# Optimization experiments

Hardware: AMD Instinct MI355X
Metric: run time of the kernel (lower is better)

Reference implementation:

```python
import jax, jax.numpy as jnp
import numpy as np

PATCH_NUMS = (1, 2, 3, 4, 5, 6, 8, 10, 13, 16)
MAX_PN = 16
N_PHI = 4
RESI_RATIO = 0.5
TOK_T = 1.0  # tokenize_temperature


def _area_matrix(n_in, n_out):
    # F.interpolate(mode='area') == adaptive_avg_pool: equal-weight fractional bins
    M = np.zeros((n_out, n_in), np.float32)
    for i in range(n_out):
        s = (i * n_in) // n_out
        e = -((-(i + 1) * n_in) // n_out)  # ceil
        M[i, s:e] = 1.0 / (e - s)
    return M


def _cubic(t, a=-0.75):
    t = abs(float(t))
    if t <= 1.0:
        return (a + 2) * t ** 3 - (a + 3) * t ** 2 + 1.0
    if t < 2.0:
        return a * t ** 3 - 5 * a * t ** 2 + 8 * a * t - 4 * a
    return 0.0


def _bicubic_matrix(n_in, n_out):
    # PyTorch bicubic, align_corners=False, a=-0.75, edge-clamped taps
    M = np.zeros((n_out, n_in), np.float32)
    scale = n_in / n_out
    for j in range(n_out):
        src = (j + 0.5) * scale - 0.5
        fi = int(np.floor(src))
        t = src - fi
        for k in range(-1, 3):
            idx = min(max(fi + k, 0), n_in - 1)
            M[j, idx] += _cubic(k - t)
    return M


def _resize_sep(x, M):
    # separable spatial resize: x [B,C,H,W] -> [B,C,out,out]
    y = jnp.einsum('ph,bchw->bcpw', M, x)
    return jnp.einsum('qw,bcpw->bcpq', M, y)


def setup_inputs() -> dict:
    key = jax.random.key(0)
    k1, k2, k3 = jax.random.split(key, 3)
    feat = jax.random.normal(k1, (128, 32, 16, 16), jnp.float32)
    codebook = jax.random.normal(k2, (4096, 32), jnp.float32)
    phi_w = jax.random.normal(k3, (N_PHI, 32, 32, 3, 3), jnp.float32) * 0.05
    phi_b = jnp.zeros((N_PHI, 32), jnp.float32)
    return {"feat": feat, "codebook": codebook, "phi_w": phi_w, "phi_b": phi_b}


def reference(feat, codebook, phi_w, phi_b):
    B, C, H, W = feat.shape
    K = len(PATCH_NUMS)
    denom = max(K - 1, 1)
    c2 = jnp.sum(codebook * codebook, axis=-1)  # [V]
    f_rest = feat
    f_hat = jnp.zeros_like(feat)
    contexts = []
    for si, pn in enumerate(PATCH_NUMS):
        if si < K - 1:
            A = jnp.asarray(_area_matrix(H, pn))
            z = _resize_sep(f_rest, A)
        else:
            z = f_rest
        zt = z.transpose(0, 2, 3, 1).reshape(B, pn * pn, C)  # [B, pn^2, C]
        x2 = jnp.sum(zt * zt, axis=-1, keepdims=True)
        logits = -(x2 + c2[None, None, :] - 2.0 * jnp.einsum('bnc,vc->bnv', zt, codebook))
        probs = jax.nn.softmax(logits / max(TOK_T, 1e-6), axis=-1)
        idx = jnp.argmax(probs, axis=-1)
        hard = codebook[idx]                                   # [B, pn^2, C]
        soft = jnp.einsum('bnv,vc->bnc', probs, codebook)
        emb = hard + soft - jax.lax.stop_gradient(soft)        # STE (fwd value == hard)
        h = emb.reshape(B, pn, pn, C).transpose(0, 3, 1, 2)    # [B, C, pn, pn]
        if si < K - 1:
            U = jnp.asarray(_bicubic_matrix(pn, MAX_PN))
            h_up = _resize_sep(h, U)
        else:
            h_up = h
        pi = int(round(si / denom * (N_PHI - 1)))              # quant_resi[si/denom]
        conv = jax.lax.conv_general_dilated(
            h_up, phi_w[pi], (1, 1), 'SAME',
            dimension_numbers=('NCHW', 'OIHW', 'NCHW')) + phi_b[pi][None, :, None, None]
        h_up = h_up * (1.0 - RESI_RATIO) + conv * RESI_RATIO
        f_hat = f_hat + h_up
        f_rest = f_rest - h_up
        if pn < MAX_PN:
            fk = _resize_sep(f_hat, jnp.asarray(_area_matrix(H, pn)))
        else:
            fk = f_hat
        contexts.append(fk.reshape(B, C, pn * pn).transpose(0, 2, 1))  # [B, pn^2, C]
    return jnp.concatenate(contexts, axis=1)  # [B, 680, C]
```

## Files before the change

### kernel.cpp

```cpp
#include <hip/hip_runtime.h>

#define B 128
#define C 32
#define HH 16
#define V 4096
#define MARGIN 1e-4f

typedef __attribute__((ext_vector_type(8))) short bf16x8;
typedef __attribute__((ext_vector_type(4))) float f32x4;


__device__ __forceinline__ float cubicw(float t) {
    float at = fabsf(t);
    float at2 = at * at, at3 = at2 * at;
    if (at <= 1.f) return 1.25f * at3 - 2.25f * at2 + 1.f;
    if (at < 2.f)  return -0.75f * at3 + 3.75f * at2 - 6.f * at + 3.f;
    return 0.f;
}

__device__ __forceinline__ unsigned short f2bf_rne(float f) {
    unsigned int u = __float_as_uint(f);
    unsigned int r = (u + 0x7fffu + ((u >> 16) & 1u)) >> 16;
    return (unsigned short)r;
}
__device__ __forceinline__ float bf2f(unsigned short h) {
    return __uint_as_float(((unsigned int)h) << 16);
}


__global__ void setup_kernel(const float* __restrict__ feat, float* __restrict__ f_rest,
                             float* __restrict__ f_hat, const float* __restrict__ cb,
                             double* __restrict__ c2d, float* __restrict__ c2f,
                             float* __restrict__ z0, unsigned short* __restrict__ cbh,
                             unsigned short* __restrict__ cbl) {
    int i = blockIdx.x * 256 + threadIdx.x;
    if (i < B * C * HH * HH) { f_rest[i] = feat[i]; f_hat[i] = 0.f; }
    if (i < V) {
        const float* p = cb + i * C;
        double s = 0.0;
        #pragma unroll
        for (int j = 0; j < C; ++j) { double d = (double)p[j]; s = fma(d, d, s); }
        c2d[i] = s;
        c2f[i] = (float)s;
    }
    if (i < B * C) {
        const float* p = feat + i * (HH * HH);
        float s = 0.f;
        for (int px = 0; px < HH * HH; ++px) s += p[px];
        z0[i] = s * (1.f / 256.f);
    }
    if (i < V * C) {
        int ii = i & 7, nn = (i >> 3) & 15, kb = (i >> 7) & 3, T = i >> 9;
        float val = cb[(T * 16 + nn) * C + kb * 8 + ii];
        unsigned short h = f2bf_rne(val);
        cbh[i] = h;
        cbl[i] = f2bf_rne(val - bf2f(h));
    }
}

__global__ __launch_bounds__(256) void scan_mfma_kernel(
    const float* __restrict__ z, const unsigned short* __restrict__ cbh,
    const unsigned short* __restrict__ cbl, const float* __restrict__ c2f,
    float4* __restrict__ pk, int npx, int nseg, int ngrp)
{
    int tid = threadIdx.x;
    int wave = tid >> 6, lane = tid & 63;
    int job = blockIdx.x * 4 + wave;
    int seg = job / ngrp, tokgrp = job - seg * ngrp;
    int cps = V / nseg;
    int total = B * npx;
    int tn = lane & 15, kb = lane >> 4;

    __shared__ float smb1[4][16 * 17];
    __shared__ float smb2[4][16 * 17];
    __shared__ int   smi1[4][16 * 17];

    bf16x8 ah, al;
    {
        int tok = tokgrp * 16 + tn;
        int bq = tok / npx, n = tok - bq * npx;
        #pragma unroll
        for (int i = 0; i < 8; ++i) {
            float v = z[(bq * C + kb * 8 + i) * npx + n];
            unsigned short h = f2bf_rne(v);
            ah[i] = (short)h;
            al[i] = (short)f2bf_rne(v - bf2f(h));
        }
    }

    const bf16x8* ph = reinterpret_cast<const bf16x8*>(cbh);
    const bf16x8* pl = reinterpret_cast<const bf16x8*>(cbl);

    float b1[4], b2[4]; int i1[4];
    #pragma unroll
    for (int s = 0; s < 4; ++s) { b1[s] = 3e38f; b2[s] = 3e38f; i1[s] = 0; }

    int T0 = seg * (cps >> 4), nT = cps >> 4;
    #pragma unroll 1
    for (int t = 0; t < nT; ++t) {
        int T = T0 + t;
        bf16x8 bh = ph[(size_t)T * 64 + lane];
        bf16x8 bl = pl[(size_t)T * 64 + lane];
        float c2v = c2f[T * 16 + tn];

        f32x4 a0 = {0.f, 0.f, 0.f, 0.f};
        a0 = __builtin_amdgcn_mfma_f32_16x16x32_bf16(ah, bh, a0, 0, 0, 0);
        a0 = __builtin_amdgcn_mfma_f32_16x16x32_bf16(al, bh, a0, 0, 0, 0);
        a0 = __builtin_amdgcn_mfma_f32_16x16x32_bf16(ah, bl, a0, 0, 0, 0);
        a0 = __builtin_amdgcn_mfma_f32_16x16x32_bf16(al, bl, a0, 0, 0, 0);

        int code = T * 16 + tn;
        #pragma unroll
        for (int r = 0; r < 4; ++r) {
            float s0 = fmaf(-2.f, a0[r], c2v);
            if (s0 < b1[r]) { b2[r] = b1[r]; b1[r] = s0; i1[r] = code; }
            else if (s0 < b2[r]) { b2[r] = s0; }
        }
    }

    #pragma unroll
    for (int r = 0; r < 4; ++r) {
        int tokl = kb * 4 + r;
        smb1[wave][tokl * 17 + tn] = b1[r];
        smb2[wave][tokl * 17 + tn] = b2[r];
        smi1[wave][tokl * 17 + tn] = i1[r];
    }
    __syncthreads();
    if (tid < 64) {
        int w = tid >> 4, tl = tid & 15;
        int jobw = blockIdx.x * 4 + w;
        int segw = jobw / ngrp, tgw = jobw - segw * ngrp;
        float gb1 = 3e38f, gb2 = 3e38f; int gi1 = 0;
        #pragma unroll
        for (int i = 0; i < 16; ++i) {
            float v1 = smb1[w][tl * 17 + i];
            int   ix = smi1[w][tl * 17 + i];
            if (v1 < gb1 || (v1 == gb1 && ix < gi1)) { gb2 = gb1; gb1 = v1; gi1 = ix; }
            else if (v1 < gb2) { gb2 = v1; }
            float v2 = smb2[w][tl * 17 + i];
            if (v2 < gb2) gb2 = v2;
        }
        int tok = tgw * 16 + tl;
        float4 o;
        o.x = gb1; o.y = gb2; o.z = __int_as_float(gi1); o.w = 0.f;
        pk[(size_t)segw * total + tok] = o;
    }
}

__global__ __launch_bounds__(256) void stage_tail_kernel(
    const float4* __restrict__ pk, const float* __restrict__ z,
    const float* __restrict__ cb, const double* __restrict__ c2d,
    const float* __restrict__ w, const float* __restrict__ bias,
    float* __restrict__ f_hat, float* __restrict__ f_rest,
    float* __restrict__ out, float* __restrict__ znext,
    int pn, int off, int pn2, int nseg)
{
    int bb = blockIdx.x >> 2;
    int og = (blockIdx.x & 3) * 8;
    int tid = threadIdx.x;
    int npx = pn * pn;
    int total = B * npx;

    __shared__ float A_s[32][257];
    __shared__ float Bc[16][257];
    __shared__ alignas(16) float w_s[8 * 384];
    __shared__ int idx_s[256];
    __shared__ int flist[256];
    __shared__ int fcnt;
    __shared__ double zsd[C];
    __shared__ double sred[256];
    __shared__ int sidx[256];
    __shared__ float wtab[16][4];
    __shared__ int   itab[16][4];
    float (*fh_s)[257] = &A_s[0];
    float (*fr_s)[257] = &A_s[8];

    float pf[8], pr[8];
    #pragma unroll
    for (int o = 0; o < 8; ++o) {
        int gi = (bb * 32 + og + o) * 256 + tid;
        pf[o] = f_hat[gi]; pr[o] = f_rest[gi];
    }
    for (int e = tid; e < 8 * 288; e += 256) {
        int o = e / 288, r = e - o * 288;
        w_s[o * 384 + (r / 9) * 12 + (r % 9)] = w[(size_t)og * 288 + e];
    }

    if (tid < 16) {
        float scale = (float)pn * (1.f / 16.f);
        float src = (tid + 0.5f) * scale - 0.5f;
        int fi = (int)floorf(src);
        float t = src - (float)fi;
        #pragma unroll
        for (int k = 0; k < 4; ++k) {
            wtab[tid][k] = cubicw((float)(k - 1) - t);
            itab[tid][k] = min(max(fi + k - 1, 0), pn - 1);
        }
    }
    if (tid == 0) fcnt = 0;
    __syncthreads();

    if (tid < npx) {
        int tok = bb * npx + tid;
        float gb1 = 3e38f, gb2 = 3e38f; int gi1 = 0;
        for (int s = 0; s < nseg; ++s) {
            float4 e = pk[(size_t)s * total + tok];
            float v1 = e.x; int ix = __float_as_int(e.z);
            if (v1 < gb1 || (v1 == gb1 && ix < gi1)) { gb2 = gb1; gb1 = v1; gi1 = ix; }
            else if (v1 < gb2) { gb2 = v1; }
            if (e.y < gb2) gb2 = e.y;
        }
        idx_s[tid] = gi1;
        if (gb2 - gb1 < MARGIN) { int slot = atomicAdd(&fcnt, 1); flist[slot] = tid; }
    }
    __syncthreads();

    int nf = fcnt;
    for (int f = 0; f < nf; ++f) {
        int n = flist[f];
        if (tid < C) zsd[tid] = (double)z[(bb * C + tid) * npx + n];
        __syncthreads();
        double best = 1e300; int bi = 0x7fffffff;
        for (int k = 0; k < V / 256; ++k) {
            int v = tid + k * 256;
            const float4* cp = reinterpret_cast<const float4*>(cb + (size_t)v * C);
            double acc = 0.0;
            #pragma unroll
            for (int qq = 0; qq < 8; ++qq) {
                float4 fv = cp[qq];
                acc = fma((double)fv.x, zsd[4 * qq + 0], acc);
                acc = fma((double)fv.y, zsd[4 * qq + 1], acc);
                acc = fma((double)fv.z, zsd[4 * qq + 2], acc);
                acc = fma((double)fv.w, zsd[4 * qq + 3], acc);
            }
            double s = fma(-2.0, acc, c2d[v]);
            if (s < best || (s == best && v < bi)) { best = s; bi = v; }
        }
        sred[tid] = best; sidx[tid] = bi;
        __syncthreads();
        for (int st = 128; st > 0; st >>= 1) {
            if (tid < st) {
                double o = sred[tid + st]; int oi = sidx[tid + st];
                double me = sred[tid];     int mi = sidx[tid];
                if (o < me || (o == me && oi < mi)) { sred[tid] = o; sidx[tid] = oi; }
            }
            __syncthreads();
        }
        if (tid == 0) idx_s[n] = sidx[0];
        __syncthreads();
    }
    __syncthreads();

    for (int e = tid; e < 32 * npx; e += 256) {
        int c = e & 31, n = e >> 5;
        A_s[c][n] = cb[idx_s[n] * 32 + c];
    }
    __syncthreads();

    #pragma unroll 1
    for (int ch = 0; ch < 2; ++ch) {
        for (int e = tid; e < 16 * 16 * pn; e += 256) {
            int wx = e % pn; int rest = e / pn;
            int p = rest & 15, cl = rest >> 4;
            float s = 0.f;
            #pragma unroll
            for (int k = 0; k < 4; ++k)
                s = fmaf(wtab[p][k], A_s[ch * 16 + cl][itab[p][k] * pn + wx], s);
            Bc[cl][p * pn + wx] = s;
        }
        __syncthreads();
        #pragma unroll
        for (int it = 0; it < 16; ++it) {
            int e = tid + it * 256;
            int q = e & 15, p = (e >> 4) & 15, cl = e >> 8;
            float s = 0.f;
            #pragma unroll
            for (int k = 0; k < 4; ++k)
                s = fmaf(wtab[q][k], Bc[cl][p * pn + itab[q][k]], s);
            A_s[ch * 16 + cl][e & 255] = s;
        }
        __syncthreads();
    }

    int p = tid >> 4, q = tid & 15;
    float acc[8];
    #pragma unroll
    for (int o = 0; o < 8; ++o) acc[o] = bias[og + o];
    for (int i = 0; i < 32; ++i) {
        float v[9];
        #pragma unroll
        for (int dy = 0; dy < 3; ++dy)
            #pragma unroll
            for (int dx = 0; dx < 3; ++dx) {
                int pp = p + dy - 1, qq = q + dx - 1;
                bool in = (pp >= 0) & (pp < 16) & (qq >= 0) & (qq < 16);
                v[dy * 3 + dx] = in ? A_s[i][pp * 16 + qq] : 0.f;
            }
        #pragma unroll
        for (int o = 0; o < 8; ++o) {
            const float* wr = &w_s[o * 384 + i * 12];
            float4 wa = *reinterpret_cast<const float4*>(wr);
            float4 wb = *reinterpret_cast<const float4*>(wr + 4);
            float w8 = wr[8];
            acc[o] = fmaf(wa.x, v[0], acc[o]); acc[o] = fmaf(wa.y, v[1], acc[o]);
            acc[o] = fmaf(wa.z, v[2], acc[o]); acc[o] = fmaf(wa.w, v[3], acc[o]);
            acc[o] = fmaf(wb.x, v[4], acc[o]); acc[o] = fmaf(wb.y, v[5], acc[o]);
            acc[o] = fmaf(wb.z, v[6], acc[o]); acc[o] = fmaf(wb.w, v[7], acc[o]);
            acc[o] = fmaf(w8,   v[8], acc[o]);
        }
    }
    float hv[8];
    #pragma unroll
    for (int o = 0; o < 8; ++o) hv[o] = A_s[og + o][tid];
    __syncthreads();

    #pragma unroll
    for (int o = 0; o < 8; ++o) {
        int gi = (bb * 32 + og + o) * 256 + tid;
        float blend = 0.5f * hv[o] + 0.5f * acc[o];
        float nf2 = pf[o] + blend;
        float nr2 = pr[o] - blend;
        f_hat[gi] = nf2; f_rest[gi] = nr2;
        fh_s[o][tid] = nf2; fr_s[o][tid] = nr2;
    }
    __syncthreads();

    for (int e = tid; e < 8 * npx; e += 256) {
        int o = e & 7, n = e >> 3;
        int y = n / pn, x = n - y * pn;
        int sh = (y * HH) / pn, eh = ((y + 1) * HH + pn - 1) / pn;
        int sw = (x * HH) / pn, ew = ((x + 1) * HH + pn - 1) / pn;
        float s = 0.f;
        for (int yy = sh; yy < eh; ++yy)
            for (int xx = sw; xx < ew; ++xx) s += fh_s[o][yy * 16 + xx];
        out[((bb * 680) + off + n) * 32 + og + o] = s * (1.f / (float)((eh - sh) * (ew - sw)));
    }

    if (pn2 > 0) {
        int npx2 = pn2 * pn2;
        for (int e = tid; e < 8 * npx2; e += 256) {
            int o = e / npx2, n = e - o * npx2;
            int y = n / pn2, x = n - y * pn2;
            int sh = (y * HH) / pn2, eh = ((y + 1) * HH + pn2 - 1) / pn2;
            int sw = (x * HH) / pn2, ew = ((x + 1) * HH + pn2 - 1) / pn2;
            float s = 0.f;
            for (int yy = sh; yy < eh; ++yy)
                for (int xx = sw; xx < ew; ++xx) s += fr_s[o][yy * 16 + xx];
            znext[(bb * 32 + og + o) * npx2 + n] = s * (1.f / (float)((eh - sh) * (ew - sw)));
        }
    }
}


extern "C" void kernel_launch(void* const* d_in, const int* in_sizes, int n_in,
                              void* d_out, int out_size, void* d_ws, size_t ws_size,
                              hipStream_t stream) {
    const float* feat = (const float*)d_in[0];
    const float* cb   = (const float*)d_in[1];
    const float* phiw = (const float*)d_in[2];
    const float* phib = (const float*)d_in[3];
    float* out = (float*)d_out;
    float* wsf = (float*)d_ws;

    const int NE = B * C * HH * HH;
    float* f_rest = wsf;
    float* f_hat  = wsf + NE;
    float* zA     = wsf + 2 * NE;
    float* zB     = wsf + 3 * NE;
    char*  tl     = (char*)(wsf + 4 * NE);
    double* c2d  = (double*)tl;
    float*  c2f  = (float*)(tl + (32 << 10));
    float4* pk   = (float4*)(tl + (48 << 10));
    unsigned short* cbh = (unsigned short*)(tl + (48 << 10) + (4 << 20));
    unsigned short* cbl = (unsigned short*)(tl + (48 << 10) + (4 << 20) + (512 << 10));

    static const int PN_[10]   = {1, 2, 3, 4, 5, 6, 8, 10, 13, 16};
    static const int PI_[10]   = {0, 0, 1, 1, 1, 2, 2, 2, 3, 3};
    static const int OFF_[10]  = {0, 1, 5, 14, 30, 55, 91, 155, 255, 424};
    static const int NSEG_[10] = {32, 32, 32, 16, 16, 16, 8, 8, 8, 8};

    setup_kernel<<<dim3((NE + 255) / 256), dim3(256), 0, stream>>>(
        feat, f_rest, f_hat, cb, c2d, c2f, zA, cbh, cbl);

    for (int si = 0; si < 10; ++si) {
        int pn = PN_[si], npx = pn * pn;
        int tokens = B * npx;
        int nseg = NSEG_[si];
        int ngrp = tokens / 16;
        int njobs = ngrp * nseg;
        float* zin  = (si & 1) ? zB : zA;
        float* zout = (si & 1) ? zA : zB;

        scan_mfma_kernel<<<dim3(njobs / 4), dim3(256), 0, stream>>>(
            zin, cbh, cbl, c2f, pk, npx, nseg, ngrp);

        int pn2 = (si < 9) ? PN_[si + 1] : 0;
        stage_tail_kernel<<<dim3(B * 4), dim3(256), 0, stream>>>(
            pk, zin, cb, c2d,
            phiw + PI_[si] * C * C * 9, phib + PI_[si] * C,
            f_hat, f_rest, out, zout, pn, OFF_[si], pn2, nseg);
    }
}
```

Before: 687.6 us.

## Unroll codebook scan by two tiles and split stage tail into eight channel groups

The scan loop now handles two codebook tiles per iteration, so more MFMA work and loads are in flight at once. The tail kernel splits output channels into groups of 4 instead of 8 and launches twice as many blocks. It shrinks shared memory by aliasing the reduction buffers onto Bc and reading conv weights directly from global memory instead of staging them in LDS. The aim is higher occupancy and parallelism, but each batch's codebook gather, argmin refinement and bicubic upsample is now repeated across twice as many blocks.

```diff
diff --git a/kernel.cpp b/kernel.cpp
--- a/kernel.cpp
+++ b/kernel.cpp
@@ -97,24 +97,35 @@
 
     int T0 = seg * (cps >> 4), nT = cps >> 4;
     #pragma unroll 1
-    for (int t = 0; t < nT; ++t) {
+    for (int t = 0; t < nT; t += 2) {
         int T = T0 + t;
-        bf16x8 bh = ph[(size_t)T * 64 + lane];
-        bf16x8 bl = pl[(size_t)T * 64 + lane];
-        float c2v = c2f[T * 16 + tn];
-
-        f32x4 a0 = {0.f, 0.f, 0.f, 0.f};
-        a0 = __builtin_amdgcn_mfma_f32_16x16x32_bf16(ah, bh, a0, 0, 0, 0);
-        a0 = __builtin_amdgcn_mfma_f32_16x16x32_bf16(al, bh, a0, 0, 0, 0);
-        a0 = __builtin_amdgcn_mfma_f32_16x16x32_bf16(ah, bl, a0, 0, 0, 0);
-        a0 = __builtin_amdgcn_mfma_f32_16x16x32_bf16(al, bl, a0, 0, 0, 0);
-
-        int code = T * 16 + tn;
+        bf16x8 bh0 = ph[(size_t)T * 64 + lane];
+        bf16x8 bl0 = pl[(size_t)T * 64 + lane];
+        bf16x8 bh1 = ph[(size_t)(T + 1) * 64 + lane];
+        bf16x8 bl1 = pl[(size_t)(T + 1) * 64 + lane];
+        float c20 = c2f[T * 16 + tn];
+        float c21 = c2f[(T + 1) * 16 + tn];
+
+        f32x4 a0 = {0.f, 0.f, 0.f, 0.f}, a1 = {0.f, 0.f, 0.f, 0.f};
+        a0 = __builtin_amdgcn_mfma_f32_16x16x32_bf16(ah, bh0, a0, 0, 0, 0);
+        a0 = __builtin_amdgcn_mfma_f32_16x16x32_bf16(al, bh0, a0, 0, 0, 0);
+        a0 = __builtin_amdgcn_mfma_f32_16x16x32_bf16(ah, bl0, a0, 0, 0, 0);
+        a0 = __builtin_amdgcn_mfma_f32_16x16x32_bf16(al, bl0, a0, 0, 0, 0);
+        a1 = __builtin_amdgcn_mfma_f32_16x16x32_bf16(ah, bh1, a1, 0, 0, 0);
+        a1 = __builtin_amdgcn_mfma_f32_16x16x32_bf16(al, bh1, a1, 0, 0, 0);
+        a1 = __builtin_amdgcn_mfma_f32_16x16x32_bf16(ah, bl1, a1, 0, 0, 0);
+        a1 = __builtin_amdgcn_mfma_f32_16x16x32_bf16(al, bl1, a1, 0, 0, 0);
+
+        int code0 = T * 16 + tn;
+        int code1 = code0 + 16;
         #pragma unroll
         for (int r = 0; r < 4; ++r) {
-            float s0 = fmaf(-2.f, a0[r], c2v);
-            if (s0 < b1[r]) { b2[r] = b1[r]; b1[r] = s0; i1[r] = code; }
+            float s0 = fmaf(-2.f, a0[r], c20);
+            if (s0 < b1[r]) { b2[r] = b1[r]; b1[r] = s0; i1[r] = code0; }
             else if (s0 < b2[r]) { b2[r] = s0; }
+            float s1 = fmaf(-2.f, a1[r], c21);
+            if (s1 < b1[r]) { b2[r] = b1[r]; b1[r] = s1; i1[r] = code1; }
+            else if (s1 < b2[r]) { b2[r] = s1; }
         }
     }
 
@@ -155,35 +166,30 @@
     float* __restrict__ out, float* __restrict__ znext,
     int pn, int off, int pn2, int nseg)
 {
-    int bb = blockIdx.x >> 2;
-    int og = (blockIdx.x & 3) * 8;
+    int bb = blockIdx.x >> 3;
+    int og = (blockIdx.x & 7) * 4;
     int tid = threadIdx.x;
     int npx = pn * pn;
     int total = B * npx;
 
     __shared__ float A_s[32][257];
-    __shared__ float Bc[16][257];
-    __shared__ alignas(16) float w_s[8 * 384];
+    __shared__ alignas(16) float Bc[4][260];
     __shared__ int idx_s[256];
     __shared__ int flist[256];
     __shared__ int fcnt;
-    __shared__ double zsd[C];
-    __shared__ double sred[256];
-    __shared__ int sidx[256];
     __shared__ float wtab[16][4];
     __shared__ int   itab[16][4];
     float (*fh_s)[257] = &A_s[0];
-    float (*fr_s)[257] = &A_s[8];
-
-    float pf[8], pr[8];
-    #pragma unroll
-    for (int o = 0; o < 8; ++o) {
+    float (*fr_s)[257] = &A_s[4];
+    double* zsd  = (double*)&Bc[0][0];
+    double* sred = (double*)((char*)&Bc[0][0] + 256);
+    int*    sidx = (int*)((char*)&Bc[0][0] + 2304);
+
+    float pf[4], pr[4];
+    #pragma unroll
+    for (int o = 0; o < 4; ++o) {
         int gi = (bb * 32 + og + o) * 256 + tid;
         pf[o] = f_hat[gi]; pr[o] = f_rest[gi];
-    }
-    for (int e = tid; e < 8 * 288; e += 256) {
-        int o = e / 288, r = e - o * 288;
-        w_s[o * 384 + (r / 9) * 12 + (r % 9)] = w[(size_t)og * 288 + e];
     }
 
     if (tid < 16) {
@@ -258,34 +264,34 @@
     __syncthreads();
 
     #pragma unroll 1
-    for (int ch = 0; ch < 2; ++ch) {
-        for (int e = tid; e < 16 * 16 * pn; e += 256) {
+    for (int ch = 0; ch < 8; ++ch) {
+        for (int e = tid; e < 4 * 16 * pn; e += 256) {
             int wx = e % pn; int rest = e / pn;
             int p = rest & 15, cl = rest >> 4;
             float s = 0.f;
             #pragma unroll
             for (int k = 0; k < 4; ++k)
-                s = fmaf(wtab[p][k], A_s[ch * 16 + cl][itab[p][k] * pn + wx], s);
+                s = fmaf(wtab[p][k], A_s[ch * 4 + cl][itab[p][k] * pn + wx], s);
             Bc[cl][p * pn + wx] = s;
         }
         __syncthreads();
         #pragma unroll
-        for (int it = 0; it < 16; ++it) {
+        for (int it = 0; it < 4; ++it) {
             int e = tid + it * 256;
             int q = e & 15, p = (e >> 4) & 15, cl = e >> 8;
             float s = 0.f;
             #pragma unroll
             for (int k = 0; k < 4; ++k)
                 s = fmaf(wtab[q][k], Bc[cl][p * pn + itab[q][k]], s);
-            A_s[ch * 16 + cl][e & 255] = s;
+            A_s[ch * 4 + cl][e & 255] = s;
         }
         __syncthreads();
     }
 
     int p = tid >> 4, q = tid & 15;
-    float acc[8];
-    #pragma unroll
-    for (int o = 0; o < 8; ++o) acc[o] = bias[og + o];
+    float acc[4];
+    #pragma unroll
+    for (int o = 0; o < 4; ++o) acc[o] = bias[og + o];
     for (int i = 0; i < 32; ++i) {
         float v[9];
         #pragma unroll
@@ -297,25 +303,19 @@
                 v[dy * 3 + dx] = in ? A_s[i][pp * 16 + qq] : 0.f;
             }
         #pragma unroll
-        for (int o = 0; o < 8; ++o) {
-            const float* wr = &w_s[o * 384 + i * 12];
-            float4 wa = *reinterpret_cast<const float4*>(wr);
-            float4 wb = *reinterpret_cast<const float4*>(wr + 4);
-            float w8 = wr[8];
-            acc[o] = fmaf(wa.x, v[0], acc[o]); acc[o] = fmaf(wa.y, v[1], acc[o]);
-            acc[o] = fmaf(wa.z, v[2], acc[o]); acc[o] = fmaf(wa.w, v[3], acc[o]);
-            acc[o] = fmaf(wb.x, v[4], acc[o]); acc[o] = fmaf(wb.y, v[5], acc[o]);
-            acc[o] = fmaf(wb.z, v[6], acc[o]); acc[o] = fmaf(wb.w, v[7], acc[o]);
-            acc[o] = fmaf(w8,   v[8], acc[o]);
-        }
-    }
-    float hv[8];
-    #pragma unroll
-    for (int o = 0; o < 8; ++o) hv[o] = A_s[og + o][tid];
-    __syncthreads();
-
-    #pragma unroll
-    for (int o = 0; o < 8; ++o) {
+        for (int o = 0; o < 4; ++o) {
+            const float* wp_ = w + ((og + o) * 32 + i) * 9;
+            #pragma unroll
+            for (int k = 0; k < 9; ++k) acc[o] = fmaf(wp_[k], v[k], acc[o]);
+        }
+    }
+    float hv[4];
+    #pragma unroll
+    for (int o = 0; o < 4; ++o) hv[o] = A_s[og + o][tid];
+    __syncthreads();
+
+    #pragma unroll
+    for (int o = 0; o < 4; ++o) {
         int gi = (bb * 32 + og + o) * 256 + tid;
         float blend = 0.5f * hv[o] + 0.5f * acc[o];
         float nf2 = pf[o] + blend;
@@ -325,8 +325,8 @@
     }
     __syncthreads();
 
-    for (int e = tid; e < 8 * npx; e += 256) {
-        int o = e & 7, n = e >> 3;
+    for (int e = tid; e < 4 * npx; e += 256) {
+        int o = e & 3, n = e >> 2;
         int y = n / pn, x = n - y * pn;
         int sh = (y * HH) / pn, eh = ((y + 1) * HH + pn - 1) / pn;
         int sw = (x * HH) / pn, ew = ((x + 1) * HH + pn - 1) / pn;
@@ -338,7 +338,7 @@
 
     if (pn2 > 0) {
         int npx2 = pn2 * pn2;
-        for (int e = tid; e < 8 * npx2; e += 256) {
+        for (int e = tid; e < 4 * npx2; e += 256) {
             int o = e / npx2, n = e - o * npx2;
             int y = n / pn2, x = n - y * pn2;
             int sh = (y * HH) / pn2, eh = ((y + 1) * HH + pn2 - 1) / pn2;
@@ -395,7 +395,7 @@
             zin, cbh, cbl, c2f, pk, npx, nseg, ngrp);
 
         int pn2 = (si < 9) ? PN_[si + 1] : 0;
-        stage_tail_kernel<<<dim3(B * 4), dim3(256), 0, stream>>>(
+        stage_tail_kernel<<<dim3(B * 8), dim3(256), 0, stream>>>(
             pk, zin, cb, c2d,
             phiw + PI_[si] * C * C * 9, phib + PI_[si] * C,
             f_hat, f_rest, out, zout, pn, OFF_[si], pn2, nseg);
```

Measured after the change: 700.2 us. No clear change (+1.8%).

## Share codebook tiles across waves via double-buffered LDS in VQ scan

Applied to the files above, without the earlier changes.

Each block's four waves now handle different token groups of the same codebook segment, so one codebook tile (hi/lo bf16 plus norms) is loaded once per block into a double-buffered LDS slot and shared, instead of each wave reading it from global memory. The next tile is prefetched while the current one is used. The segment counts per stage are also retuned, with more segments at pn=4 and fewer at the two largest stages. This cuts global and L2 traffic for the codebook but adds a block-wide barrier every iteration, and only a few threads issue the loads.

```diff
diff --git a/kernel.cpp b/kernel.cpp
--- a/kernel.cpp
+++ b/kernel.cpp
@@ -61,23 +61,25 @@
 __global__ __launch_bounds__(256) void scan_mfma_kernel(
     const float* __restrict__ z, const unsigned short* __restrict__ cbh,
     const unsigned short* __restrict__ cbl, const float* __restrict__ c2f,
-    float4* __restrict__ pk, int npx, int nseg, int ngrp)
+    float4* __restrict__ pk, int npx, int nseg, int nblk_tok)
 {
     int tid = threadIdx.x;
     int wave = tid >> 6, lane = tid & 63;
-    int job = blockIdx.x * 4 + wave;
-    int seg = job / ngrp, tokgrp = job - seg * ngrp;
+    int tb  = blockIdx.x % nblk_tok;
+    int seg = blockIdx.x / nblk_tok;
     int cps = V / nseg;
     int total = B * npx;
     int tn = lane & 15, kb = lane >> 4;
 
+    __shared__ alignas(16) float4 ldsB[2][128];
+    __shared__ float ldsc2[2][16];
     __shared__ float smb1[4][16 * 17];
     __shared__ float smb2[4][16 * 17];
     __shared__ int   smi1[4][16 * 17];
 
     bf16x8 ah, al;
     {
-        int tok = tokgrp * 16 + tn;
+        int tok = (tb * 4 + wave) * 16 + tn;
         int bq = tok / npx, n = tok - bq * npx;
         #pragma unroll
         for (int i = 0; i < 8; ++i) {
@@ -88,20 +90,33 @@
         }
     }
 
-    const bf16x8* ph = reinterpret_cast<const bf16x8*>(cbh);
-    const bf16x8* pl = reinterpret_cast<const bf16x8*>(cbl);
+    const float4* phv = reinterpret_cast<const float4*>(cbh);
+    const float4* plv = reinterpret_cast<const float4*>(cbl);
 
     float b1[4], b2[4]; int i1[4];
     #pragma unroll
     for (int s = 0; s < 4; ++s) { b1[s] = 3e38f; b2[s] = 3e38f; i1[s] = 0; }
 
     int T0 = seg * (cps >> 4), nT = cps >> 4;
+
+    if (tid < 64)       ldsB[0][tid]       = phv[(size_t)T0 * 64 + tid];
+    else if (tid < 128) ldsB[0][tid]       = plv[(size_t)T0 * 64 + (tid - 64)];
+    else if (tid < 144) ldsc2[0][tid - 128] = c2f[T0 * 16 + (tid - 128)];
+    __syncthreads();
+
     #pragma unroll 1
     for (int t = 0; t < nT; ++t) {
-        int T = T0 + t;
-        bf16x8 bh = ph[(size_t)T * 64 + lane];
-        bf16x8 bl = pl[(size_t)T * 64 + lane];
-        float c2v = c2f[T * 16 + tn];
+        int cur = t & 1, nxt = cur ^ 1;
+        if (t + 1 < nT) {
+            int Tn = T0 + t + 1;
+            if (tid < 64)       ldsB[nxt][tid]        = phv[(size_t)Tn * 64 + tid];
+            else if (tid < 128) ldsB[nxt][tid]        = plv[(size_t)Tn * 64 + (tid - 64)];
+            else if (tid < 144) ldsc2[nxt][tid - 128] = c2f[Tn * 16 + (tid - 128)];
+        }
+
+        bf16x8 bh = *reinterpret_cast<const bf16x8*>(&ldsB[cur][lane]);
+        bf16x8 bl = *reinterpret_cast<const bf16x8*>(&ldsB[cur][64 + lane]);
+        float c2v = ldsc2[cur][tn];
 
         f32x4 a0 = {0.f, 0.f, 0.f, 0.f};
         a0 = __builtin_amdgcn_mfma_f32_16x16x32_bf16(ah, bh, a0, 0, 0, 0);
@@ -109,13 +124,14 @@
         a0 = __builtin_amdgcn_mfma_f32_16x16x32_bf16(ah, bl, a0, 0, 0, 0);
         a0 = __builtin_amdgcn_mfma_f32_16x16x32_bf16(al, bl, a0, 0, 0, 0);
 
-        int code = T * 16 + tn;
+        int code = (T0 + t) * 16 + tn;
         #pragma unroll
         for (int r = 0; r < 4; ++r) {
             float s0 = fmaf(-2.f, a0[r], c2v);
             if (s0 < b1[r]) { b2[r] = b1[r]; b1[r] = s0; i1[r] = code; }
             else if (s0 < b2[r]) { b2[r] = s0; }
         }
+        __syncthreads();
     }
 
     #pragma unroll
@@ -128,8 +144,6 @@
     __syncthreads();
     if (tid < 64) {
         int w = tid >> 4, tl = tid & 15;
-        int jobw = blockIdx.x * 4 + w;
-        int segw = jobw / ngrp, tgw = jobw - segw * ngrp;
         float gb1 = 3e38f, gb2 = 3e38f; int gi1 = 0;
         #pragma unroll
         for (int i = 0; i < 16; ++i) {
@@ -140,10 +154,10 @@
             float v2 = smb2[w][tl * 17 + i];
             if (v2 < gb2) gb2 = v2;
         }
-        int tok = tgw * 16 + tl;
+        int tok = (tb * 4 + w) * 16 + tl;
         float4 o;
         o.x = gb1; o.y = gb2; o.z = __int_as_float(gi1); o.w = 0.f;
-        pk[(size_t)segw * total + tok] = o;
+        pk[(size_t)seg * total + tok] = o;
     }
 }
 
@@ -377,7 +391,7 @@
     static const int PN_[10]   = {1, 2, 3, 4, 5, 6, 8, 10, 13, 16};
     static const int PI_[10]   = {0, 0, 1, 1, 1, 2, 2, 2, 3, 3};
     static const int OFF_[10]  = {0, 1, 5, 14, 30, 55, 91, 155, 255, 424};
-    static const int NSEG_[10] = {32, 32, 32, 16, 16, 16, 8, 8, 8, 8};
+    static const int NSEG_[10] = {32, 32, 32, 32, 16, 16, 8, 8, 4, 4};
 
     setup_kernel<<<dim3((NE + 255) / 256), dim3(256), 0, stream>>>(
         feat, f_rest, f_hat, cb, c2d, c2f, zA, cbh, cbl);
@@ -386,13 +400,13 @@
         int pn = PN_[si], npx = pn * pn;
         int tokens = B * npx;
         int nseg = NSEG_[si];
-        int ngrp = tokens / 16;
-        int njobs = ngrp * nseg;
+        int nblk_tok = tokens / 64;
+        int nblk = nblk_tok * nseg;
         float* zin  = (si & 1) ? zB : zA;
         float* zout = (si & 1) ? zA : zB;
 
-        scan_mfma_kernel<<<dim3(njobs / 4), dim3(256), 0, stream>>>(
-            zin, cbh, cbl, c2f, pk, npx, nseg, ngrp);
+        scan_mfma_kernel<<<dim3(nblk), dim3(256), 0, stream>>>(
+            zin, cbh, cbl, c2f, pk, npx, nseg, nblk_tok);
 
         int pn2 = (si < 9) ? PN_[si + 1] : 0;
         stage_tail_kernel<<<dim3(B * 4), dim3(256), 0, stream>>>(
```

Result: slower. 726.9 us (+5.7%).
